# Kernel optimization log

Measured on AMD Instinct MI355X. Metric: run time of the kernel, lower is better.

## Reference

```python
import jax, jax.numpy as jnp
import numpy as np
import math

EMBED_DIM = 1024
NUM_HEADS = 4
HEAD_DIM = EMBED_DIM // NUM_HEADS
B, N = 4, 2048


def setup_inputs() -> dict:
    key = jax.random.key(0)
    ks = jax.random.split(key, 5)
    s = 1.0 / math.sqrt(EMBED_DIM)
    return {
        "x": jax.random.normal(ks[0], (B, N, EMBED_DIM), dtype=jnp.float32),
        "w_qkv": jax.random.normal(ks[1], (EMBED_DIM, 3 * EMBED_DIM), dtype=jnp.float32) * s,
        "b_qkv": jnp.zeros((3 * EMBED_DIM,), dtype=jnp.float32),
        "w_out": jax.random.normal(ks[2], (EMBED_DIM, EMBED_DIM), dtype=jnp.float32) * s,
        "b_out": jnp.zeros((EMBED_DIM,), dtype=jnp.float32),
        "ln_gamma": jnp.ones((EMBED_DIM,), dtype=jnp.float32),
        "ln_beta": jnp.zeros((EMBED_DIM,), dtype=jnp.float32),
    }


def reference(x, w_qkv, b_qkv, w_out, b_out, ln_gamma, ln_beta):
    Bx, Nx, D = x.shape
    qkv = x @ w_qkv + b_qkv  # [B, N, 3D]
    q, k, v = jnp.split(qkv, 3, axis=-1)
    # [B, H, N, hd]
    def heads(t):
        return t.reshape(Bx, Nx, NUM_HEADS, HEAD_DIM).transpose(0, 2, 1, 3)
    q, k, v = heads(q), heads(k), heads(v)
    scale = 1.0 / math.sqrt(HEAD_DIM)
    attn = jnp.einsum("bhqd,bhkd->bhqk", q, k) * scale  # [B, H, N, N]
    attn = jax.nn.softmax(attn, axis=-1)
    out = jnp.einsum("bhqk,bhkd->bhqd", attn, v)  # [B, H, N, hd]
    out = out.transpose(0, 2, 1, 3).reshape(Bx, Nx, D)
    out = out @ w_out + b_out
    # residual + LayerNorm (eps=1e-5 like torch default)
    y = x + out
    mu = jnp.mean(y, axis=-1, keepdims=True)
    var = jnp.mean(jnp.square(y - mu), axis=-1, keepdims=True)
    y = (y - mu) * jax.lax.rsqrt(var + 1e-5)
    return y * ln_gamma + ln_beta
```

## Files before the change

kernel.cpp:

```cpp
#include <hip/hip_runtime.h>
#include <hip/hip_bf16.h>

typedef __attribute__((ext_vector_type(8))) short short8;
typedef __attribute__((ext_vector_type(4))) float f32x4;
typedef __attribute__((ext_vector_type(16))) float f32x16;
typedef __attribute__((ext_vector_type(4))) unsigned uint4v;

#define GLOB_AS __attribute__((address_space(1)))
#define LDS_AS  __attribute__((address_space(3)))

__device__ __forceinline__ void async16(void* lds, const void* g) {
  __builtin_amdgcn_global_load_lds((const GLOB_AS unsigned int*)g,
                                   (LDS_AS unsigned int*)lds, 16, 0, 0);
}

__device__ __forceinline__ unsigned short f2bf(float f) {
  unsigned u = __float_as_uint(f);
  unsigned r = u + 0x7FFFu + ((u >> 16) & 1u);
  return (unsigned short)(r >> 16);
}

__device__ __forceinline__ float bf2f(unsigned short u) {
  unsigned x = ((unsigned)u) << 16;
  return __uint_as_float(x);
}

__device__ __forceinline__ unsigned pk2(float lo, float hi) {
  __hip_bfloat162 h = __float22bfloat162_rn(float2{lo, hi});
  return *reinterpret_cast<unsigned*>(&h);
}

__device__ __forceinline__ void lane32_swap(unsigned& a, unsigned& b, int lane) {
#if __has_builtin(__builtin_amdgcn_permlane32_swap)
  auto r = __builtin_amdgcn_permlane32_swap(a, b, false, false);
  a = r[0]; b = r[1];
#else
  unsigned tb = __shfl_xor(b, 32);
  unsigned ta = __shfl_xor(a, 32);
  unsigned na = (lane < 32) ? a : tb;
  unsigned nb = (lane < 32) ? ta : b;
  a = na; b = nb;
#endif
}

#define BATCH 4
#define SEQ   2048
#define DMODEL 1024
#define NHEAD 4
#define HD    256

#define QSCALE 0.090169944f
#define DEFER_THR 11.5f

__global__ __launch_bounds__(256) void cast_bf16_kernel(
    const float* __restrict__ in, unsigned short* __restrict__ out) {
  int i = blockIdx.x * 256 + threadIdx.x;
  float4 v = ((const float4*)in)[i];
  uint2 o;
  o.x = (unsigned)f2bf(v.x) | ((unsigned)f2bf(v.y) << 16);
  o.y = (unsigned)f2bf(v.z) | ((unsigned)f2bf(v.w) << 16);
  ((uint2*)out)[i] = o;
}

__global__ __launch_bounds__(256) void transpose_cast_kernel(
    const float* __restrict__ in, unsigned short* __restrict__ out, int R, int C) {
  __shared__ float tile[32][33];
  int c0 = blockIdx.x * 32, r0 = blockIdx.y * 32;
  int tx = threadIdx.x, ty = threadIdx.y;
#pragma unroll
  for (int i = 0; i < 4; ++i)
    tile[ty + 8 * i][tx] = in[(size_t)(r0 + ty + 8 * i) * C + c0 + tx];
  __syncthreads();
#pragma unroll
  for (int i = 0; i < 4; ++i)
    out[(size_t)(c0 + ty + 8 * i) * R + r0 + tx] = f2bf(tile[tx][ty + 8 * i]);
}

__global__ __launch_bounds__(256) void gemm_qkv_kernel(
    const unsigned short* __restrict__ A,
    const unsigned short* __restrict__ Bt,
    const float* __restrict__ bias,
    unsigned short* __restrict__ qb,
    unsigned short* __restrict__ kb,
    unsigned short* __restrict__ vt) {
  __shared__ __align__(16) unsigned short sA[128 * 32];
  __shared__ __align__(16) unsigned short sB[128 * 32];
  const int t = threadIdx.x;
  const int l = t & 63, w = t >> 6;
  const int g = l >> 4, lr = l & 15;
  const int wr = w >> 1, wc = w & 1;
  const int row0 = blockIdx.y * 128;
  const int col0 = blockIdx.x * 128;

  f32x4 acc[4][4] = {};
  for (int kt = 0; kt < 1024; kt += 32) {
    __syncthreads();
#pragma unroll
    for (int i = 0; i < 2; ++i) {
      int e = i * 256 + t;
      async16(&sA[e * 8], A + (size_t)(row0 + (e >> 2)) * 1024 + kt + (e & 3) * 8);
      async16(&sB[e * 8], Bt + (size_t)(col0 + (e >> 2)) * 1024 + kt + (e & 3) * 8);
    }
    __syncthreads();
    short8 af[4], bf[4];
#pragma unroll
    for (int m = 0; m < 4; ++m)
      af[m] = *(const short8*)&sA[(wr * 64 + m * 16 + lr) * 32 + g * 8];
#pragma unroll
    for (int n = 0; n < 4; ++n)
      bf[n] = *(const short8*)&sB[(wc * 64 + n * 16 + lr) * 32 + g * 8];
#pragma unroll
    for (int m = 0; m < 4; ++m)
#pragma unroll
      for (int n = 0; n < 4; ++n)
        acc[m][n] = __builtin_amdgcn_mfma_f32_16x16x32_bf16(af[m], bf[n], acc[m][n], 0, 0, 0);
  }

#pragma unroll
  for (int m = 0; m < 4; ++m) {
    int rowb = row0 + wr * 64 + m * 16 + g * 4;
    int b = rowb >> 11;
    int nb = rowb & 2047;
#pragma unroll
    for (int nn = 0; nn < 4; ++nn) {
      int col = col0 + wc * 64 + nn * 16 + lr;
      float bv = bias[col];
      int sec = col >> 10, c1 = col & 1023;
      int h = c1 >> 8, d = c1 & 255;
      if (sec == 2) {
        unsigned short p0 = f2bf(acc[m][nn][0] + bv);
        unsigned short p1 = f2bf(acc[m][nn][1] + bv);
        unsigned short p2 = f2bf(acc[m][nn][2] + bv);
        unsigned short p3 = f2bf(acc[m][nn][3] + bv);
        uint2 pk;
        pk.x = (unsigned)p0 | ((unsigned)p1 << 16);
        pk.y = (unsigned)p2 | ((unsigned)p3 << 16);
        size_t idx = (((size_t)((b * NHEAD + h) * 128 + (nb >> 4))) * 256 + d) * 16 + (nb & 15);
        *(uint2*)&vt[idx] = pk;
      } else {
        unsigned short* dst = (sec == 0) ? qb : kb;
        float sc = (sec == 0) ? QSCALE : 1.0f;
#pragma unroll
        for (int rr = 0; rr < 4; ++rr) {
          size_t idx = ((size_t)((b * NHEAD + h) * SEQ + nb + rr)) * HD + d;
          dst[idx] = f2bf((acc[m][nn][rr] + bv) * sc);
        }
      }
    }
  }
}

__global__ __launch_bounds__(256, 2) void attn_kernel(
    const unsigned short* __restrict__ qb,
    const unsigned short* __restrict__ kb,
    const unsigned short* __restrict__ vt,
    unsigned short* __restrict__ Oh,
    float2* __restrict__ st) {
  __shared__ __align__(16) unsigned short sK[2][32 * 256];
  __shared__ __align__(16) unsigned short sV[2][2 * 256 * 16];
  const int t = threadIdx.x, l = t & 63, w = t >> 6;
  const int row = l & 31, hi = l >> 5;
  const int swz = (row & 7) << 4;
  const int bid = blockIdx.x;
  const int bh = (bid & 7) * 2 + ((bid >> 3) & 1);
  const int qblk = (bid >> 4) & 15;
  const int kvhalf = bid >> 8;
  const int b = bh >> 2, h = bh & 3;
  const int q = qblk * 128 + w * 32 + row;
  const unsigned short* Qp = qb + (size_t)bh * SEQ * HD;
  const char* Kg = (const char*)(kb + (size_t)bh * SEQ * HD);
  const char* Vg = (const char*)(vt + (size_t)bh * (128 * 256 * 16));

  short8 qf[16];
#pragma unroll
  for (int dc = 0; dc < 16; ++dc)
    qf[dc] = *(const short8*)&Qp[(size_t)q * HD + dc * 16 + hi * 8];

  auto stage = [&](int buf, int kp0) {
#pragma unroll
    for (int i = 0; i < 4; ++i) {
      int s = i * 256 + t;
      int r = s >> 5;
      int colb = (s & 31) * 16;
      int src = (kp0 + r) * 512 + (colb ^ ((r & 7) << 4));
      async16((char*)sK[buf] + s * 16, Kg + src);
    }
    const int c0 = kp0 >> 4;
#pragma unroll
    for (int i = 0; i < 4; ++i) {
      int s = i * 256 + t;
      int kh = s >> 9, rem = s & 511;
      int d = rem >> 1, vhi = rem & 1;
      int src = ((c0 + kh) * 256 + d) * 32 + vhi * 16;
      async16((char*)sV[buf] + s * 16, Vg + src);
    }
  };

  stage(0, kvhalf * 32);
  __syncthreads();

  f32x16 O[8] = {};
  float mrun = -__builtin_inff();
  float lsum = 0.f;

  for (int it = 0; it < 32; ++it) {
    const int kp0 = (2 * it + kvhalf) * 32;
    const int cur = it & 1;
    if (it < 31) stage(cur ^ 1, kp0 + 64);

    f32x16 Sa = {}, Sb = {};
    const char* sKc = (const char*)sK[cur];
    __builtin_amdgcn_s_setprio(1);
#pragma unroll
    for (int dc = 0; dc < 16; dc += 2) {
      short8 kf0 = *(const short8*)(sKc + row * 512 + ((dc * 32 + hi * 16) ^ swz));
      short8 kf1 = *(const short8*)(sKc + row * 512 + (((dc + 1) * 32 + hi * 16) ^ swz));
      Sa = __builtin_amdgcn_mfma_f32_32x32x16_bf16(kf0, qf[dc], Sa, 0, 0, 0);
      Sb = __builtin_amdgcn_mfma_f32_32x32x16_bf16(kf1, qf[dc + 1], Sb, 0, 0, 0);
    }
    __builtin_amdgcn_s_setprio(0);

    float p[16];
#pragma unroll
    for (int i = 0; i < 16; ++i) p[i] = Sa[i] + Sb[i];
    float m0 = fmaxf(fmaxf(fmaxf(p[0], p[1]), fmaxf(p[2], p[3])),
                     fmaxf(fmaxf(p[4], p[5]), fmaxf(p[6], p[7])));
    float m1 = fmaxf(fmaxf(fmaxf(p[8], p[9]), fmaxf(p[10], p[11])),
                     fmaxf(fmaxf(p[12], p[13]), fmaxf(p[14], p[15])));
    float cmax = fmaxf(m0, m1);
    cmax = fmaxf(cmax, __shfl_xor(cmax, 32));

    if (!__all(cmax <= mrun + DEFER_THR)) {
      float mnew = fmaxf(mrun, cmax);
      float alpha = exp2f(mrun - mnew);
      lsum *= alpha;
#pragma unroll
      for (int db = 0; db < 8; ++db) O[db] *= alpha;
      mrun = mnew;
    }

    float e[16];
#pragma unroll
    for (int i = 0; i < 16; ++i) e[i] = exp2f(p[i] - mrun);
    float s0 = (e[0] + e[1]) + (e[2] + e[3]);
    float s1 = (e[4] + e[5]) + (e[6] + e[7]);
    float s2 = (e[8] + e[9]) + (e[10] + e[11]);
    float s3 = (e[12] + e[13]) + (e[14] + e[15]);
    float ps = (s0 + s1) + (s2 + s3);
    ps += __shfl_xor(ps, 32);
    lsum += ps;

    unsigned a0 = pk2(e[0], e[1]),   a1 = pk2(e[2], e[3]);
    unsigned b0 = pk2(e[4], e[5]),   b1 = pk2(e[6], e[7]);
    unsigned c0 = pk2(e[8], e[9]),   c1 = pk2(e[10], e[11]);
    unsigned d0 = pk2(e[12], e[13]), d1 = pk2(e[14], e[15]);
    lane32_swap(a0, b0, l);
    lane32_swap(a1, b1, l);
    lane32_swap(c0, d0, l);
    lane32_swap(c1, d1, l);
    uint4v u1; u1.x = a0; u1.y = a1; u1.z = b0; u1.w = b1;
    uint4v u2; u2.x = c0; u2.y = c1; u2.z = d0; u2.w = d1;
    short8 pf1 = __builtin_bit_cast(short8, u1);
    short8 pf2 = __builtin_bit_cast(short8, u2);

    const char* sVc = (const char*)sV[cur];
    __builtin_amdgcn_s_setprio(1);
#pragma unroll
    for (int db = 0; db < 8; ++db) {
      short8 vf0 = *(const short8*)(sVc + ((db * 32 + row) * 2 + hi) * 16);
      short8 vf1 = *(const short8*)(sVc + 8192 + ((db * 32 + row) * 2 + hi) * 16);
      O[db] = __builtin_amdgcn_mfma_f32_32x32x16_bf16(vf0, pf1, O[db], 0, 0, 0);
      O[db] = __builtin_amdgcn_mfma_f32_32x32x16_bf16(vf1, pf2, O[db], 0, 0, 0);
    }
    __builtin_amdgcn_s_setprio(0);

    __syncthreads();
  }

  float inv = 1.0f / lsum;
  unsigned short* aop = Oh + (size_t)kvhalf * (8192ull * 1024);
  size_t obase = ((size_t)(b * SEQ + q)) * DMODEL + h * HD;
#pragma unroll
  for (int db = 0; db < 8; ++db)
#pragma unroll
    for (int rg = 0; rg < 4; ++rg) {
      int dd = db * 32 + rg * 8 + hi * 4;
      uint2 pk;
      pk.x = pk2(O[db][rg * 4 + 0] * inv, O[db][rg * 4 + 1] * inv);
      pk.y = pk2(O[db][rg * 4 + 2] * inv, O[db][rg * 4 + 3] * inv);
      *(uint2*)&aop[obase + dd] = pk;
    }
  if (hi == 0)
    st[((size_t)kvhalf * 16 + bh) * 2048 + q] = make_float2(mrun, lsum);
}

__global__ __launch_bounds__(256) void combine_kernel(
    const unsigned short* __restrict__ Oh,
    const float2* __restrict__ st,
    unsigned short* __restrict__ ao) {
  int rowg = blockIdx.x, t = threadIdx.x;
  int b = rowg >> 11, q = rowg & 2047;
  int col = t * 4;
  int bh = b * 4 + (col >> 8);
  float2 s0 = st[(size_t)bh * 2048 + q];
  float2 s1 = st[(16ull * 2048) + (size_t)bh * 2048 + q];
  float M = fmaxf(s0.x, s1.x);
  float w0 = s0.y * exp2f(s0.x - M);
  float w1 = s1.y * exp2f(s1.x - M);
  float inv = 1.0f / (w0 + w1);
  w0 *= inv; w1 *= inv;
  size_t base = (size_t)rowg * 1024 + col;
  uint2 ua = *(const uint2*)&Oh[base];
  uint2 ub = *(const uint2*)&Oh[8192ull * 1024 + base];
  unsigned short oa[4] = {(unsigned short)(ua.x & 0xFFFF), (unsigned short)(ua.x >> 16),
                          (unsigned short)(ua.y & 0xFFFF), (unsigned short)(ua.y >> 16)};
  unsigned short ob[4] = {(unsigned short)(ub.x & 0xFFFF), (unsigned short)(ub.x >> 16),
                          (unsigned short)(ub.y & 0xFFFF), (unsigned short)(ub.y >> 16)};
  float r[4];
#pragma unroll
  for (int j = 0; j < 4; ++j) r[j] = w0 * bf2f(oa[j]) + w1 * bf2f(ob[j]);
  uint2 pk;
  pk.x = pk2(r[0], r[1]);
  pk.y = pk2(r[2], r[3]);
  *(uint2*)&ao[base] = pk;
}

__global__ __launch_bounds__(256) void gemm_out_kernel(
    const unsigned short* __restrict__ A,
    const unsigned short* __restrict__ Bt,
    const float* __restrict__ bias,
    const float* __restrict__ x,
    float* __restrict__ y) {
  __shared__ __align__(16) unsigned short sA[128 * 32];
  __shared__ __align__(16) unsigned short sB[128 * 32];
  const int t = threadIdx.x;
  const int l = t & 63, w = t >> 6;
  const int g = l >> 4, lr = l & 15;
  const int wr = w >> 1, wc = w & 1;
  const int row0 = blockIdx.y * 128;
  const int col0 = blockIdx.x * 128;

  f32x4 acc[4][4] = {};
  for (int kt = 0; kt < 1024; kt += 32) {
    __syncthreads();
#pragma unroll
    for (int i = 0; i < 2; ++i) {
      int e = i * 256 + t;
      async16(&sA[e * 8], A + (size_t)(row0 + (e >> 2)) * 1024 + kt + (e & 3) * 8);
      async16(&sB[e * 8], Bt + (size_t)(col0 + (e >> 2)) * 1024 + kt + (e & 3) * 8);
    }
    __syncthreads();
    short8 af[4], bf[4];
#pragma unroll
    for (int m = 0; m < 4; ++m)
      af[m] = *(const short8*)&sA[(wr * 64 + m * 16 + lr) * 32 + g * 8];
#pragma unroll
    for (int n = 0; n < 4; ++n)
      bf[n] = *(const short8*)&sB[(wc * 64 + n * 16 + lr) * 32 + g * 8];
#pragma unroll
    for (int m = 0; m < 4; ++m)
#pragma unroll
      for (int n = 0; n < 4; ++n)
        acc[m][n] = __builtin_amdgcn_mfma_f32_16x16x32_bf16(af[m], bf[n], acc[m][n], 0, 0, 0);
  }

#pragma unroll
  for (int m = 0; m < 4; ++m) {
    int rowb = row0 + wr * 64 + m * 16 + g * 4;
#pragma unroll
    for (int nn = 0; nn < 4; ++nn) {
      int col = col0 + wc * 64 + nn * 16 + lr;
      float bv = bias[col];
#pragma unroll
      for (int rr = 0; rr < 4; ++rr) {
        size_t idx = (size_t)(rowb + rr) * 1024 + col;
        y[idx] = acc[m][nn][rr] + bv + x[idx];
      }
    }
  }
}

__global__ __launch_bounds__(256) void ln_kernel(
    const float* __restrict__ y, const float* __restrict__ gamma,
    const float* __restrict__ beta, float* __restrict__ out) {
  int row = blockIdx.x, t = threadIdx.x;
  float4 v = ((const float4*)(y + (size_t)row * 1024))[t];
  float s = v.x + v.y + v.z + v.w;
  float qs = v.x * v.x + v.y * v.y + v.z * v.z + v.w * v.w;
#pragma unroll
  for (int off = 1; off < 64; off <<= 1) {
    s += __shfl_xor(s, off);
    qs += __shfl_xor(qs, off);
  }
  __shared__ float ss[4], qq[4];
  if ((t & 63) == 0) { ss[t >> 6] = s; qq[t >> 6] = qs; }
  __syncthreads();
  s = ss[0] + ss[1] + ss[2] + ss[3];
  qs = qq[0] + qq[1] + qq[2] + qq[3];
  float mean = s * (1.0f / 1024.0f);
  float var = qs * (1.0f / 1024.0f) - mean * mean;
  float rstd = rsqrtf(var + 1e-5f);
  float4 gm = ((const float4*)gamma)[t];
  float4 bt = ((const float4*)beta)[t];
  float4 o;
  o.x = (v.x - mean) * rstd * gm.x + bt.x;
  o.y = (v.y - mean) * rstd * gm.y + bt.y;
  o.z = (v.z - mean) * rstd * gm.z + bt.z;
  o.w = (v.w - mean) * rstd * gm.w + bt.w;
  ((float4*)(out + (size_t)row * 1024))[t] = o;
}

extern "C" void kernel_launch(void* const* d_in, const int* in_sizes, int n_in,
                              void* d_out, int out_size, void* d_ws, size_t ws_size,
                              hipStream_t stream) {
  const float* x      = (const float*)d_in[0];
  const float* w_qkv  = (const float*)d_in[1];
  const float* b_qkv  = (const float*)d_in[2];
  const float* w_out  = (const float*)d_in[3];
  const float* b_out  = (const float*)d_in[4];
  const float* gamma  = (const float*)d_in[5];
  const float* beta   = (const float*)d_in[6];
  float* out = (float*)d_out;

  char* ws = (char*)d_ws;
  unsigned short* xb    = (unsigned short*)(ws);
  unsigned short* wqkvT = (unsigned short*)(ws + (16u << 20));
  unsigned short* woutT = (unsigned short*)(ws + (22u << 20));
  unsigned short* qb    = (unsigned short*)(ws + (24u << 20));
  unsigned short* kb    = (unsigned short*)(ws + (40u << 20));
  unsigned short* vt    = (unsigned short*)(ws + (56u << 20));
  unsigned short* ao    = (unsigned short*)(ws + (72u << 20));
  unsigned short* Oh    = (unsigned short*)(ws + (88u << 20));
  float* y              = (float*)(ws + (88u << 20));
  float2* st            = (float2*)(ws + (16u << 20));

  cast_bf16_kernel<<<(BATCH * SEQ * DMODEL) / (256 * 4), 256, 0, stream>>>(x, xb);
  transpose_cast_kernel<<<dim3(96, 32), dim3(32, 8), 0, stream>>>(w_qkv, wqkvT, 1024, 3072);
  transpose_cast_kernel<<<dim3(32, 32), dim3(32, 8), 0, stream>>>(w_out, woutT, 1024, 1024);
  gemm_qkv_kernel<<<dim3(24, 64), 256, 0, stream>>>(xb, wqkvT, b_qkv, qb, kb, vt);
  attn_kernel<<<512, 256, 0, stream>>>(qb, kb, vt, Oh, st);
  combine_kernel<<<BATCH * SEQ, 256, 0, stream>>>(Oh, st, ao);
  gemm_out_kernel<<<dim3(8, 64), 256, 0, stream>>>(ao, woutT, b_out, x, y);
  ln_kernel<<<BATCH * SEQ, 256, 0, stream>>>(y, gamma, beta, out);
}
```

Baseline: 244.7 us.

## Double-buffer GEMM LDS tiles, raise MFMA priority, widen attention K swizzle

Both projection GEMMs (QKV and output) now keep two LDS buffers. The next K-slice is issued with async global-to-LDS loads right after the barrier, so it streams in while the current slice feeds the MFMAs, and each iteration needs one barrier instead of two. The MFMA block is wrapped in s_setprio so waves doing matrix math get priority over waves issuing loads. The attention kernel's K-tile XOR swizzle now uses all 32 row bits instead of row&7, meant to spread LDS bank access more widely. The cost is double the LDS per GEMM block, which could lower occupancy, and the wider swizzle is only correct if every K read in the attention kernel applies the same swz value.

New measurement: 248.9 us. Within noise of the previous version (+1.7%).

```diff
diff --git a/kernel.cpp b/kernel.cpp
--- a/kernel.cpp
+++ b/kernel.cpp
@@ -83,8 +83,8 @@
     unsigned short* __restrict__ qb,
     unsigned short* __restrict__ kb,
     unsigned short* __restrict__ vt) {
-  __shared__ __align__(16) unsigned short sA[128 * 32];
-  __shared__ __align__(16) unsigned short sB[128 * 32];
+  __shared__ __align__(16) unsigned short sA[2][128 * 32];
+  __shared__ __align__(16) unsigned short sB[2][128 * 32];
   const int t = threadIdx.x;
   const int l = t & 63, w = t >> 6;
   const int g = l >> 4, lr = l & 15;
@@ -92,28 +92,36 @@
   const int row0 = blockIdx.y * 128;
   const int col0 = blockIdx.x * 128;
 
-  f32x4 acc[4][4] = {};
-  for (int kt = 0; kt < 1024; kt += 32) {
-    __syncthreads();
+  auto stage = [&](int buf, int kt) {
 #pragma unroll
     for (int i = 0; i < 2; ++i) {
       int e = i * 256 + t;
-      async16(&sA[e * 8], A + (size_t)(row0 + (e >> 2)) * 1024 + kt + (e & 3) * 8);
-      async16(&sB[e * 8], Bt + (size_t)(col0 + (e >> 2)) * 1024 + kt + (e & 3) * 8);
-    }
+      async16(&sA[buf][e * 8], A + (size_t)(row0 + (e >> 2)) * 1024 + kt + (e & 3) * 8);
+      async16(&sB[buf][e * 8], Bt + (size_t)(col0 + (e >> 2)) * 1024 + kt + (e & 3) * 8);
+    }
+  };
+
+  stage(0, 0);
+
+  f32x4 acc[4][4] = {};
+  for (int ki = 0; ki < 32; ++ki) {
+    const int cur = ki & 1;
     __syncthreads();
+    if (ki < 31) stage(cur ^ 1, (ki + 1) * 32);
     short8 af[4], bf[4];
 #pragma unroll
     for (int m = 0; m < 4; ++m)
-      af[m] = *(const short8*)&sA[(wr * 64 + m * 16 + lr) * 32 + g * 8];
+      af[m] = *(const short8*)&sA[cur][(wr * 64 + m * 16 + lr) * 32 + g * 8];
 #pragma unroll
     for (int n = 0; n < 4; ++n)
-      bf[n] = *(const short8*)&sB[(wc * 64 + n * 16 + lr) * 32 + g * 8];
+      bf[n] = *(const short8*)&sB[cur][(wc * 64 + n * 16 + lr) * 32 + g * 8];
+    __builtin_amdgcn_s_setprio(1);
 #pragma unroll
     for (int m = 0; m < 4; ++m)
 #pragma unroll
       for (int n = 0; n < 4; ++n)
         acc[m][n] = __builtin_amdgcn_mfma_f32_16x16x32_bf16(af[m], bf[n], acc[m][n], 0, 0, 0);
+    __builtin_amdgcn_s_setprio(0);
   }
 
 #pragma unroll
@@ -160,7 +168,7 @@
   __shared__ __align__(16) unsigned short sV[2][2 * 256 * 16];
   const int t = threadIdx.x, l = t & 63, w = t >> 6;
   const int row = l & 31, hi = l >> 5;
-  const int swz = (row & 7) << 4;
+  const int swz = row << 4;
   const int bid = blockIdx.x;
   const int bh = (bid & 7) * 2 + ((bid >> 3) & 1);
   const int qblk = (bid >> 4) & 15;
@@ -182,7 +190,7 @@
       int s = i * 256 + t;
       int r = s >> 5;
       int colb = (s & 31) * 16;
-      int src = (kp0 + r) * 512 + (colb ^ ((r & 7) << 4));
+      int src = (kp0 + r) * 512 + (colb ^ (r << 4));
       async16((char*)sK[buf] + s * 16, Kg + src);
     }
     const int c0 = kp0 >> 4;
@@ -331,8 +339,8 @@
     const float* __restrict__ bias,
     const float* __restrict__ x,
     float* __restrict__ y) {
-  __shared__ __align__(16) unsigned short sA[128 * 32];
-  __shared__ __align__(16) unsigned short sB[128 * 32];
+  __shared__ __align__(16) unsigned short sA[2][128 * 32];
+  __shared__ __align__(16) unsigned short sB[2][128 * 32];
   const int t = threadIdx.x;
   const int l = t & 63, w = t >> 6;
   const int g = l >> 4, lr = l & 15;
@@ -340,28 +348,36 @@
   const int row0 = blockIdx.y * 128;
   const int col0 = blockIdx.x * 128;
 
-  f32x4 acc[4][4] = {};
-  for (int kt = 0; kt < 1024; kt += 32) {
-    __syncthreads();
+  auto stage = [&](int buf, int kt) {
 #pragma unroll
     for (int i = 0; i < 2; ++i) {
       int e = i * 256 + t;
-      async16(&sA[e * 8], A + (size_t)(row0 + (e >> 2)) * 1024 + kt + (e & 3) * 8);
-      async16(&sB[e * 8], Bt + (size_t)(col0 + (e >> 2)) * 1024 + kt + (e & 3) * 8);
-    }
+      async16(&sA[buf][e * 8], A + (size_t)(row0 + (e >> 2)) * 1024 + kt + (e & 3) * 8);
+      async16(&sB[buf][e * 8], Bt + (size_t)(col0 + (e >> 2)) * 1024 + kt + (e & 3) * 8);
+    }
+  };
+
+  stage(0, 0);
+
+  f32x4 acc[4][4] = {};
+  for (int ki = 0; ki < 32; ++ki) {
+    const int cur = ki & 1;
     __syncthreads();
+    if (ki < 31) stage(cur ^ 1, (ki + 1) * 32);
     short8 af[4], bf[4];
 #pragma unroll
     for (int m = 0; m < 4; ++m)
-      af[m] = *(const short8*)&sA[(wr * 64 + m * 16 + lr) * 32 + g * 8];
+      af[m] = *(const short8*)&sA[cur][(wr * 64 + m * 16 + lr) * 32 + g * 8];
 #pragma unroll
     for (int n = 0; n < 4; ++n)
-      bf[n] = *(const short8*)&sB[(wc * 64 + n * 16 + lr) * 32 + g * 8];
+      bf[n] = *(const short8*)&sB[cur][(wc * 64 + n * 16 + lr) * 32 + g * 8];
+    __builtin_amdgcn_s_setprio(1);
 #pragma unroll
     for (int m = 0; m < 4; ++m)
 #pragma unroll
       for (int n = 0; n < 4; ++n)
         acc[m][n] = __builtin_amdgcn_mfma_f32_16x16x32_bf16(af[m], bf[n], acc[m][n], 0, 0, 0);
+    __builtin_amdgcn_s_setprio(0);
   }
 
 #pragma unroll
```
